# Kernel tuning notes

Hardware: AMD Instinct MI355X
Metric: run time of the kernel (lower is better)

The kernel has to match this reference:

```python
import jax, jax.numpy as jnp
import numpy as np

B, S, HIDDEN = 1, 2048, 3584
NH, NKV, HD = 16, 8, 256
N_REP = NH // NKV
EPS = 1e-6
SCALING = 256.0 ** -0.5  # query_pre_attn_scalar=256
SOFTCAP = 50.0
NEG = -1e9


def rmsnorm(x, w):
    # Gemma RMSNorm with unit offset, computed in fp32
    xf = x.astype(jnp.float32)
    n = xf * jax.lax.rsqrt(jnp.mean(xf * xf, axis=-1, keepdims=True) + EPS)
    return (n * (1.0 + w.astype(jnp.float32))).astype(x.dtype)


def rope(x, cos, sin):
    # x: [B,S,H,D]; gemma pairs (x[:D/2], x[D/2:]) as complex (rotate-half)
    x1, x2 = jnp.split(x, 2, axis=-1)
    c = cos[None, :, None, :]
    s = sin[None, :, None, :]
    return jnp.concatenate([x1 * c - x2 * s, x1 * s + x2 * c], axis=-1).astype(x.dtype)


def setup_inputs() -> dict:
    key = jax.random.key(0)
    ks = jax.random.split(key, 6)
    hidden_states = jax.random.normal(ks[0], (B, S, HIDDEN), jnp.float32)
    w_qkv = jax.random.normal(ks[1], ((NH + 2 * NKV) * HD, HIDDEN), jnp.float32) * 0.02
    w_o = jax.random.normal(ks[2], (HIDDEN, NH * HD), jnp.float32) * 0.02
    q_norm_w = jax.random.normal(ks[3], (HD,), jnp.float32) * 0.1
    k_norm_w = jax.random.normal(ks[4], (HD,), jnp.float32) * 0.1
    k_cache = jnp.zeros((B, S, NKV, HD), jnp.float32)
    v_cache = jnp.zeros((B, S, NKV, HD), jnp.float32)
    kv_write_indices = jnp.arange(S, dtype=jnp.int32)
    # rotary tables, theta=10000
    inv_freq = 1.0 / (10000.0 ** (np.arange(0, HD, 2, dtype=np.float32) / HD))
    t = np.arange(S, dtype=np.float32)
    freqs = np.outer(t, inv_freq)  # [S, HD/2]
    cos = jnp.asarray(np.cos(freqs), jnp.float32)
    sin = jnp.asarray(np.sin(freqs), jnp.float32)
    # causal additive mask [1,1,S,S]
    causal = np.tril(np.ones((S, S), dtype=bool))
    mask = jnp.asarray(np.where(causal, 0.0, NEG).astype(np.float32))[None, None]
    return {"hidden_states": hidden_states, "cos": cos, "sin": sin,
            "kv_write_indices": kv_write_indices, "k_cache": k_cache,
            "v_cache": v_cache, "mask": mask, "w_qkv": w_qkv, "w_o": w_o,
            "q_norm_w": q_norm_w, "k_norm_w": k_norm_w}


def reference(hidden_states, cos, sin, kv_write_indices, k_cache, v_cache,
              mask, w_qkv, w_o, q_norm_w, k_norm_w):
    qkv = jnp.einsum('bsh,oh->bso', hidden_states, w_qkv)
    q_size, kv_size = NH * HD, NKV * HD
    xq = qkv[..., :q_size].reshape(B, S, NH, HD)
    xk = qkv[..., q_size:q_size + kv_size].reshape(B, S, NKV, HD)
    xv = qkv[..., q_size + kv_size:].reshape(B, S, NKV, HD)
    xq = rmsnorm(xq, q_norm_w)
    xk = rmsnorm(xk, k_norm_w)
    xq = rope(xq, cos, sin)
    xk = rope(xk, cos, sin)
    # KV cache write (index_copy_ along dim 1)
    kc = k_cache.at[:, kv_write_indices].set(xk)
    vc = v_cache.at[:, kv_write_indices].set(xv)
    # GQA expand
    key = jnp.repeat(kc, N_REP, axis=2)   # [B,S,NH,HD]
    val = jnp.repeat(vc, N_REP, axis=2)
    q = xq.transpose(0, 2, 1, 3) * SCALING  # [B,NH,S,HD]
    k = key.transpose(0, 2, 1, 3)
    v = val.transpose(0, 2, 1, 3)
    scores = jnp.einsum('bhqd,bhkd->bhqk', q, k)
    scores = jnp.tanh(scores / SOFTCAP) * SOFTCAP  # logit softcapping
    scores = scores + mask
    p = jax.nn.softmax(scores, axis=-1)
    out = jnp.einsum('bhqk,bhkd->bhqd', p, v)
    out = out.transpose(0, 2, 1, 3).reshape(B, S, NH * HD)
    return jnp.einsum('bsd,hd->bsh', out, w_o)
```

## Files before the change

kernel.cpp:

```cpp
#include <hip/hip_runtime.h>

typedef __bf16 bf16;
typedef __bf16 bf16x4 __attribute__((ext_vector_type(4)));
typedef __bf16 bf16x8 __attribute__((ext_vector_type(8)));
typedef float f32x4 __attribute__((ext_vector_type(4)));

#define S_LEN 2048
#define HID   3584
#define NHEADS 16
#define NKVH   8
#define HDIM   256
#define QKV_O  8192
#define O_IN   4096

typedef const __attribute__((address_space(1))) void* gp_t;
typedef __attribute__((address_space(3))) void* sp_t;

__device__ __forceinline__ void async16(const void* g, void* s) {
  __builtin_amdgcn_global_load_lds((gp_t)g, (sp_t)s, 16, 0, 0);
}

__device__ __forceinline__ f32x4 mfma16(bf16x8 a, bf16x8 b, f32x4 c) {
  return __builtin_amdgcn_mfma_f32_16x16x32_bf16(a, b, c, 0, 0, 0);
}

__global__ __launch_bounds__(256) void cast_kernel(const float* __restrict__ in,
                                                   bf16* __restrict__ out, int n4) {
  int i = blockIdx.x * 256 + threadIdx.x;
  if (i >= n4) return;
  f32x4 v = ((const f32x4*)in)[i];
  bf16x4 o = { (bf16)v[0], (bf16)v[1], (bf16)v[2], (bf16)v[3] };
  ((bf16x4*)out)[i] = o;
}

__global__ __launch_bounds__(256) void add2_kernel(const float* __restrict__ a,
                                                   const float* __restrict__ b,
                                                   float* __restrict__ o, int n4) {
  int i = blockIdx.x * 256 + threadIdx.x;
  if (i >= n4) return;
  f32x4 x = ((const f32x4*)a)[i];
  f32x4 y = ((const f32x4*)b)[i];
  ((f32x4*)o)[i] = x + y;
}

#define GSTG(gb, lb, kk, half, LDAB) do {                              \
    const bf16* _g = (gb) + (size_t)((half) * 128) * (LDAB) + (kk);    \
    bf16* _l = (lb) + (half) * 128 * 64 + soff;                        \
    async16(_g, _l);                                                   \
    async16(_g + (size_t)64 * (LDAB), _l + 64 * 64);                   \
  } while (0)
#define LD12(ab, bb, cx, ar, br) do {                                  \
    const bf16* _pa = (ab) + arow;                                     \
    const bf16* _pb = (bb) + brow;                                     \
    _Pragma("unroll")                                                  \
    for (int _i = 0; _i < 8; _i++) ar[_i] = *(const bf16x8*)(_pa + _i * 16 * 64 + (cx)); \
    _Pragma("unroll")                                                  \
    for (int _j = 0; _j < 4; _j++) br[_j] = *(const bf16x8*)(_pb + _j * 16 * 64 + (cx)); \
  } while (0)
#define MM32(ar, br) do {                                              \
    __builtin_amdgcn_s_setprio(1);                                     \
    _Pragma("unroll")                                                  \
    for (int _i = 0; _i < 8; _i++)                                     \
      _Pragma("unroll")                                                \
      for (int _j = 0; _j < 4; _j++)                                   \
        acc[_i][_j] = mfma16(ar[_i], br[_j], acc[_i][_j]);             \
    __builtin_amdgcn_s_setprio(0);                                     \
  } while (0)
#define BARS() do { __builtin_amdgcn_s_barrier(); __builtin_amdgcn_sched_barrier(0); } while (0)
#define LGKM0() asm volatile("s_waitcnt lgkmcnt(0)" ::: "memory")
#define WAITV8() asm volatile("s_waitcnt vmcnt(8)" ::: "memory")

#define GEMM_PIPE_BODY(LDAB)                                           \
  f32x4 acc[8][4];                                                     \
  _Pragma("unroll")                                                    \
  for (int i = 0; i < 8; i++)                                          \
    _Pragma("unroll")                                                  \
    for (int j = 0; j < 4; j++) { f32x4 z = {0.f, 0.f, 0.f, 0.f}; acc[i][j] = z; } \
  bf16x8 a0[8], b0[4], a1[8], b1[4];                                   \
  const int nT = K >> 6;                                               \
  const int nIter = K >> 7;                                            \
  GSTG(Ag, As0, 0, 0, LDAB); GSTG(Ag, As0, 0, 1, LDAB);                \
  GSTG(Bg, Bs0, 0, 0, LDAB); GSTG(Bg, Bs0, 0, 1, LDAB);                \
  GSTG(Ag, As1, 64, 0, LDAB); GSTG(Ag, As1, 64, 1, LDAB);              \
  GSTG(Bg, Bs1, 64, 0, LDAB); GSTG(Bg, Bs1, 64, 1, LDAB);              \
  WAITV8();                                                            \
  BARS();                                                              \
  LD12(As0, Bs0, c0, a0, b0);                                          \
  for (int t = 0; t < nIter; t++) {                                    \
    int t2 = 2 * t + 2; if (t2 > nT - 1) t2 = nT - 1;                  \
    int t3 = 2 * t + 3; if (t3 > nT - 1) t3 = nT - 1;                  \
    int k2 = t2 * 64, k3 = t3 * 64;                                    \
              \
    LD12(As0, Bs0, c1, a1, b1);                                        \
    MM32(a0, b0);                                                      \
    LGKM0();                                                           \
    BARS();                                                            \
    \
    GSTG(Ag, As0, k2, 0, LDAB); GSTG(Ag, As0, k2, 1, LDAB);            \
    GSTG(Bg, Bs0, k2, 0, LDAB); GSTG(Bg, Bs0, k2, 1, LDAB);            \
    MM32(a1, b1);                                                      \
    WAITV8();                                                          \
    BARS();                                                            \
    LD12(As1, Bs1, c0, a0, b0);                                        \
                                             \
    LD12(As1, Bs1, c1, a1, b1);                                        \
    MM32(a0, b0);                                                      \
    LGKM0();                                                           \
    BARS();                                                            \
                                                              \
    GSTG(Ag, As1, k3, 0, LDAB); GSTG(Ag, As1, k3, 1, LDAB);            \
    GSTG(Bg, Bs1, k3, 0, LDAB); GSTG(Bg, Bs1, k3, 1, LDAB);            \
    MM32(a1, b1);                                                      \
    WAITV8();                                                          \
    BARS();                                                            \
    LD12(As0, Bs0, c0, a0, b0);                                        \
  }

__global__ __launch_bounds__(512, 2) void gemm_nt_8p(const bf16* __restrict__ A,
                                                     const bf16* __restrict__ B,
                                                     float* __restrict__ C,
                                                     int M, int N, int K) {
  __shared__ bf16 As0[256 * 64];
  __shared__ bf16 Bs0[256 * 64];
  __shared__ bf16 As1[256 * 64];
  __shared__ bf16 Bs1[256 * 64];
  int tid = threadIdx.x;
  int lane = tid & 63;
  int w = tid >> 6;
  int wm = w >> 2, wn = w & 3;
  int lid = blockIdx.x;
  int oid = (lid & 7) * 32 + (lid >> 3);
  int rect = oid >> 5, ri = oid & 31;
  int bm = (rect & 3) * 2 + (ri >> 4);
  int bn = (rect >> 2) * 16 + (ri & 15);
  int srow = tid >> 3, schunk = tid & 7;
  int gcol = (schunk ^ (srow & 7)) * 8;
  const bf16* Ag = A + (size_t)(bm * 256 + srow) * K + gcol;
  const bf16* Bg = B + (size_t)(bn * 256 + srow) * K + gcol;
  int soff = srow * 64 + schunk * 8;
  int fr = lane & 15, fq = lane >> 4;
  int c0 = ((fq) ^ (fr & 7)) * 8;
  int c1 = ((4 + fq) ^ (fr & 7)) * 8;
  const int arow = (wm * 128 + fr) * 64;
  const int brow = (wn * 64 + fr) * 64;

  GEMM_PIPE_BODY(K)

  int row0 = bm * 256 + wm * 128 + fq * 4;
  int col0 = bn * 256 + wn * 64 + fr;
#pragma unroll
  for (int i = 0; i < 8; i++)
#pragma unroll
    for (int j = 0; j < 4; j++)
#pragma unroll
      for (int r = 0; r < 4; r++)
        C[(size_t)(row0 + i * 16 + r) * N + col0 + j * 16] = acc[i][j][r];
}

__global__ __launch_bounds__(512, 2) void gemm_nt_8p_ks(const bf16* __restrict__ A,
                                                        const bf16* __restrict__ B,
                                                        float* __restrict__ C,
                                                        int M, int N, int K, int lda) {
  __shared__ bf16 As0[256 * 64];
  __shared__ bf16 Bs0[256 * 64];
  __shared__ bf16 As1[256 * 64];
  __shared__ bf16 Bs1[256 * 64];
  int tid = threadIdx.x;
  int lane = tid & 63;
  int w = tid >> 6;
  int wm = w >> 2, wn = w & 3;
  int lid = blockIdx.x;
  int ks = lid >= 112;
  int l2 = lid - ks * 112;
  int oid = (l2 & 7) * 14 + (l2 >> 3);
  int bm = oid / 14;
  int bn = oid - bm * 14;
  int kbase = ks * K;
  float* Cp = C + (size_t)ks * M * N;
  int srow = tid >> 3, schunk = tid & 7;
  int gcol = (schunk ^ (srow & 7)) * 8;
  const bf16* Ag = A + (size_t)(bm * 256 + srow) * lda + kbase + gcol;
  const bf16* Bg = B + (size_t)(bn * 256 + srow) * lda + kbase + gcol;
  int soff = srow * 64 + schunk * 8;
  int fr = lane & 15, fq = lane >> 4;
  int c0 = ((fq) ^ (fr & 7)) * 8;
  int c1 = ((4 + fq) ^ (fr & 7)) * 8;
  const int arow = (wm * 128 + fr) * 64;
  const int brow = (wn * 64 + fr) * 64;

  GEMM_PIPE_BODY(lda)

  int row0 = bm * 256 + wm * 128 + fq * 4;
  int col0 = bn * 256 + wn * 64 + fr;
#pragma unroll
  for (int i = 0; i < 8; i++)
#pragma unroll
    for (int j = 0; j < 4; j++)
#pragma unroll
      for (int r = 0; r < 4; r++)
        Cp[(size_t)(row0 + i * 16 + r) * N + col0 + j * 16] = acc[i][j][r];
}

__global__ __launch_bounds__(256) void qk_norm_rope(const float* __restrict__ qkv,
                                                    const float* __restrict__ cosb,
                                                    const float* __restrict__ sinb,
                                                    const float* __restrict__ qw,
                                                    const float* __restrict__ kw,
                                                    bf16* __restrict__ qout,
                                                    bf16* __restrict__ kout) {
  int s = blockIdx.x;
  int lane = threadIdx.x & 63;
  int w = threadIdx.x >> 6;
  int d0 = lane * 4;
  int dr = d0 & 127;
  f32x4 cv = *(const f32x4*)(cosb + s * 128 + dr);
  f32x4 sv = *(const f32x4*)(sinb + s * 128 + dr);
  bool hi = lane >= 32;
#pragma unroll
  for (int r = 0; r < 6; r++) {
    int head = r * 4 + w;
    const float* x = qkv + (size_t)s * QKV_O + head * HDIM + d0;
    f32x4 v = *(const f32x4*)x;
    float ss = v[0] * v[0] + v[1] * v[1] + v[2] * v[2] + v[3] * v[3];
#pragma unroll
    for (int off = 32; off > 0; off >>= 1) ss += __shfl_xor(ss, off);
    float scale = rsqrtf(ss * (1.0f / HDIM) + 1e-6f);
    bool isq = head < NHEADS;
    const float* wn = isq ? qw : kw;
    f32x4 wv = *(const f32x4*)(wn + d0);
    float y[4], o[4];
#pragma unroll
    for (int i = 0; i < 4; i++) y[i] = v[i] * scale * (1.0f + wv[i]);
#pragma unroll
    for (int i = 0; i < 4; i++) {
      float py = __shfl_xor(y[i], 32);
      o[i] = hi ? (py * sv[i] + y[i] * cv[i]) : (y[i] * cv[i] - py * sv[i]);
    }
    float mult = isq ? 0.0625f : 1.0f;
    bf16x4 ov = { (bf16)(o[0] * mult), (bf16)(o[1] * mult), (bf16)(o[2] * mult), (bf16)(o[3] * mult) };
    if (isq) *(bf16x4*)(qout + ((size_t)head * S_LEN + s) * HDIM + d0) = ov;
    else     *(bf16x4*)(kout + ((size_t)(head - NHEADS) * S_LEN + s) * HDIM + d0) = ov;
  }
}

__global__ __launch_bounds__(256) void v_transpose(const float* __restrict__ qkv, bf16* __restrict__ vt) {
  __shared__ float tile[64][65];
  int dt = blockIdx.x, st = blockIdx.y, h = blockIdx.z;
  int t = threadIdx.x;
  int d0 = dt * 64, s0 = st * 64;
#pragma unroll
  for (int i = 0; i < 16; i++) {
    int idx = i * 256 + t;
    int r = idx >> 6, c = idx & 63;
    tile[r][c] = qkv[(size_t)(s0 + r) * QKV_O + 6144 + h * HDIM + d0 + c];
  }
  __syncthreads();
#pragma unroll
  for (int i = 0; i < 16; i++) {
    int idx = i * 256 + t;
    int dr = idx >> 6, sc = idx & 63;
    vt[((size_t)h * HDIM + d0 + dr) * S_LEN + s0 + sc] = (bf16)tile[sc][dr];
  }
}

#define PSTRIDE 40
__global__ __launch_bounds__(256) void attn_kernel(const bf16* __restrict__ q,
                                                   const bf16* __restrict__ kx,
                                                   const bf16* __restrict__ vt,
                                                   bf16* __restrict__ aout) {
  __shared__ bf16 kt[32 * 256];
  __shared__ bf16 vtile[256 * 32];
  __shared__ bf16 pbuf[4][16 * PSTRIDE];
  int h = blockIdx.x;
  int y = blockIdx.y;
  int qt = (y < 16) ? y : 47 - y;
  int kvh = h >> 1;
  int tid = threadIdx.x;
  int lane = tid & 63, w = tid >> 6;
  int fr = lane & 15, fq = lane >> 4;
  int qs = qt * 64;
  bf16x8 qf[8];
  const bf16* qb = q + ((size_t)h * S_LEN + qs + w * 16 + fr) * HDIM + fq * 8;
#pragma unroll
  for (int i = 0; i < 8; i++) qf[i] = *(const bf16x8*)(qb + i * 32);
  f32x4 acc[16];
#pragma unroll
  for (int i = 0; i < 16; i++) { f32x4 z = {0.f, 0.f, 0.f, 0.f}; acc[i] = z; }
  float lsum[4] = {0.f, 0.f, 0.f, 0.f};
  int krow = w * 2 + (lane >> 5);
  int kcolr = (lane & 31) * 8;
  const bf16* kg = kx + (size_t)kvh * S_LEN * HDIM;
  int vd = w * 16 + (lane >> 2);
  int vsw = (vd >> 1) & 3;
  int vcl = (lane & 3) * 8;
  int vcg = (((lane & 3) ^ vsw) * 8);
  const bf16* vg = vt + (size_t)kvh * HDIM * S_LEN;
  int rot0 = (fq * 8 - fr * 8) & 255;
  int rot1 = (fq * 8 - fr * 8 - 128) & 255;
  const bf16* kt0 = &kt[fr * 256];
  const bf16* kt1 = &kt[(16 + fr) * 256];
  int fsw = (fr >> 1) & 3;
  int kmax = qs + 64;
  for (int k0 = 0; k0 < kmax; k0 += 32) {
    __syncthreads();
#pragma unroll
    for (int p = 0; p < 4; p++) {
      int r = p * 8 + krow;
      int gc = (kcolr + r * 8) & 255;
      async16(kg + (size_t)(k0 + r) * HDIM + gc, &kt[r * 256 + kcolr]);
      int d = p * 64 + vd;
      async16(vg + (size_t)d * S_LEN + k0 + vcg, &vtile[d * 32 + vcl]);
    }
    __syncthreads();
    f32x4 s0 = {0.f, 0.f, 0.f, 0.f}, s1 = {0.f, 0.f, 0.f, 0.f};
#pragma unroll
    for (int kk = 0; kk < 8; kk++) {
      bf16x8 b0 = *(const bf16x8*)(kt0 + ((kk * 32 + rot0) & 255));
      bf16x8 b1 = *(const bf16x8*)(kt1 + ((kk * 32 + rot1) & 255));
      s0 = mfma16(qf[kk], b0, s0);
      s1 = mfma16(qf[kk], b1, s1);
    }
#pragma unroll
    for (int reg = 0; reg < 4; reg++) {
      int rowg = qs + w * 16 + fq * 4 + reg;
      float u0 = __builtin_amdgcn_exp2f(0.057707802f * s0[reg]);
      float u1 = __builtin_amdgcn_exp2f(0.057707802f * s1[reg]);
      float p0 = __builtin_amdgcn_exp2f(28.853901f - 144.26950f * __builtin_amdgcn_rcpf(u0 + 1.0f));
      float p1 = __builtin_amdgcn_exp2f(28.853901f - 144.26950f * __builtin_amdgcn_rcpf(u1 + 1.0f));
      p0 = (k0 + fr <= rowg) ? p0 : 0.0f;
      p1 = (k0 + 16 + fr <= rowg) ? p1 : 0.0f;
      lsum[reg] += p0 + p1;
      pbuf[w][(fq * 4 + reg) * PSTRIDE + fr] = (bf16)p0;
      pbuf[w][(fq * 4 + reg) * PSTRIDE + 16 + fr] = (bf16)p1;
    }
    bf16x8 pf = *(const bf16x8*)&pbuf[w][fr * PSTRIDE + fq * 8];
#pragma unroll
    for (int ct = 0; ct < 16; ct++) {
      bf16x8 vf = *(const bf16x8*)&vtile[(ct * 16 + fr) * 32 + (fq ^ fsw) * 8];
      acc[ct] = mfma16(pf, vf, acc[ct]);
    }
  }
  float rl[4];
#pragma unroll
  for (int reg = 0; reg < 4; reg++) {
    float l = lsum[reg];
    l += __shfl_xor(l, 1);
    l += __shfl_xor(l, 2);
    l += __shfl_xor(l, 4);
    l += __shfl_xor(l, 8);
    rl[reg] = 1.0f / l;
  }
#pragma unroll
  for (int ct = 0; ct < 16; ct++)
#pragma unroll
    for (int reg = 0; reg < 4; reg++)
      aout[(size_t)(qs + w * 16 + fq * 4 + reg) * O_IN + h * HDIM + ct * 16 + fr] =
          (bf16)(acc[ct][reg] * rl[reg]);
}

extern "C" void kernel_launch(void* const* d_in, const int* in_sizes, int n_in,
                              void* d_out, int out_size, void* d_ws, size_t ws_size,
                              hipStream_t stream) {
  const float* hidden = (const float*)d_in[0];
  const float* cosb   = (const float*)d_in[1];
  const float* sinb   = (const float*)d_in[2];
  const float* wqkv   = (const float*)d_in[7];
  const float* wo     = (const float*)d_in[8];
  const float* qnw    = (const float*)d_in[9];
  const float* knw    = (const float*)d_in[10];
  float* out = (float*)d_out;
  char* ws = (char*)d_ws;
  bf16*  h_bf    = (bf16*)(ws + 0);
  bf16*  wqkv_bf = (bf16*)(ws + 14680064);
  bf16*  wo_bf   = (bf16*)(ws + 73400320);
  float* qkv     = (float*)(ws + 102760448);
  bf16*  qb      = (bf16*)(ws + 169869312);
  bf16*  kb      = (bf16*)(ws + 186646528);
  bf16*  vtb     = (bf16*)(ws + 195035136);
  bf16*  attnb   = (bf16*)(ws + 203423744);
  float* part0   = (float*)(ws + 102760448);
  float* part1   = part0 + (size_t)2048 * 3584;

  cast_kernel<<<7168, 256, 0, stream>>>(hidden, h_bf, 1835008);
  cast_kernel<<<28672, 256, 0, stream>>>(wqkv, wqkv_bf, 7340032);
  cast_kernel<<<14336, 256, 0, stream>>>(wo, wo_bf, 3670016);
  gemm_nt_8p<<<256, 512, 0, stream>>>(h_bf, wqkv_bf, qkv, 2048, 8192, 3584);
  qk_norm_rope<<<2048, 256, 0, stream>>>(qkv, cosb, sinb, qnw, knw, qb, kb);
  v_transpose<<<dim3(4, 32, 8), 256, 0, stream>>>(qkv, vtb);
  attn_kernel<<<dim3(16, 32), 256, 0, stream>>>(qb, kb, vtb, attnb);
  gemm_nt_8p_ks<<<224, 512, 0, stream>>>(attnb, wo_bf, part0, 2048, 3584, 2048, 4096);
  add2_kernel<<<7168, 256, 0, stream>>>(part0, part1, out, 1835008);
}
```

Measured before the change: 580.0 us.

## Double-buffer K/V tiles in attention kernel with async prefetch and MFMA priority

The attention kernel now keeps two LDS buffers for the K and V tiles. It issues the async global-to-LDS loads for the next 32-key block before computing on the current one, using a partial vmcnt wait to overlap memory with MFMA work. It also raises wave priority around the MFMA loops and requests two blocks per CU through launch_bounds. The cost is twice the LDS footprint per block, around 66KB, which may limit occupancy and conflicts with the two-blocks-per-CU target on a 160KB LDS CU. The hand-written waitcnt and barriers also risk ordering errors.

```diff
diff --git a/kernel.cpp b/kernel.cpp
--- a/kernel.cpp
+++ b/kernel.cpp
@@ -95,7 +95,7 @@
     MM32(a0, b0);                                                      \
     LGKM0();                                                           \
     BARS();                                                            \
-    \
+                                \
     GSTG(Ag, As0, k2, 0, LDAB); GSTG(Ag, As0, k2, 1, LDAB);            \
     GSTG(Bg, Bs0, k2, 0, LDAB); GSTG(Bg, Bs0, k2, 1, LDAB);            \
     MM32(a1, b1);                                                      \
@@ -264,12 +264,12 @@
 }
 
 #define PSTRIDE 40
-__global__ __launch_bounds__(256) void attn_kernel(const bf16* __restrict__ q,
-                                                   const bf16* __restrict__ kx,
-                                                   const bf16* __restrict__ vt,
-                                                   bf16* __restrict__ aout) {
-  __shared__ bf16 kt[32 * 256];
-  __shared__ bf16 vtile[256 * 32];
+__global__ __launch_bounds__(256, 2) void attn_kernel(const bf16* __restrict__ q,
+                                                      const bf16* __restrict__ kx,
+                                                      const bf16* __restrict__ vt,
+                                                      bf16* __restrict__ aout) {
+  __shared__ bf16 kt[2][32 * 256];
+  __shared__ bf16 vtile[2][256 * 32];
   __shared__ bf16 pbuf[4][16 * PSTRIDE];
   int h = blockIdx.x;
   int y = blockIdx.y;
@@ -297,22 +297,41 @@
   const bf16* vg = vt + (size_t)kvh * HDIM * S_LEN;
   int rot0 = (fq * 8 - fr * 8) & 255;
   int rot1 = (fq * 8 - fr * 8 - 128) & 255;
-  const bf16* kt0 = &kt[fr * 256];
-  const bf16* kt1 = &kt[(16 + fr) * 256];
   int fsw = (fr >> 1) & 3;
   int kmax = qs + 64;
-  for (int k0 = 0; k0 < kmax; k0 += 32) {
-    __syncthreads();
-#pragma unroll
-    for (int p = 0; p < 4; p++) {
-      int r = p * 8 + krow;
-      int gc = (kcolr + r * 8) & 255;
-      async16(kg + (size_t)(k0 + r) * HDIM + gc, &kt[r * 256 + kcolr]);
-      int d = p * 64 + vd;
-      async16(vg + (size_t)d * S_LEN + k0 + vcg, &vtile[d * 32 + vcl]);
+
+#define ASTG(KK, B) do {                                                   \
+    bf16* _kb = &kt[(B)][0]; bf16* _vb = &vtile[(B)][0];                   \
+    _Pragma("unroll")                                                      \
+    for (int p = 0; p < 4; p++) {                                          \
+      int r = p * 8 + krow;                                                \
+      int gc = (kcolr + r * 8) & 255;                                      \
+      async16(kg + (size_t)((KK) + r) * HDIM + gc, _kb + r * 256 + kcolr); \
+      int d = p * 64 + vd;                                                 \
+      async16(vg + (size_t)d * S_LEN + (KK) + vcg, _vb + d * 32 + vcl);    \
+    }                                                                      \
+  } while (0)
+
+  ASTG(0, 0);
+  int ib = 0;
+  for (int k0 = 0; k0 < kmax; k0 += 32, ib ^= 1) {
+    __builtin_amdgcn_s_barrier();
+    __builtin_amdgcn_sched_barrier(0);
+    if (k0 + 32 < kmax) {
+      ASTG(k0 + 32, ib ^ 1);
+      asm volatile("s_waitcnt vmcnt(8)" ::: "memory");
+    } else {
+      asm volatile("s_waitcnt vmcnt(0)" ::: "memory");
     }
-    __syncthreads();
+    __builtin_amdgcn_sched_barrier(0);
+    __builtin_amdgcn_s_barrier();
+    __builtin_amdgcn_sched_barrier(0);
+    const bf16* ktb = &kt[ib][0];
+    const bf16* vtb = &vtile[ib][0];
+    const bf16* kt0 = ktb + fr * 256;
+    const bf16* kt1 = ktb + (16 + fr) * 256;
     f32x4 s0 = {0.f, 0.f, 0.f, 0.f}, s1 = {0.f, 0.f, 0.f, 0.f};
+    __builtin_amdgcn_s_setprio(1);
 #pragma unroll
     for (int kk = 0; kk < 8; kk++) {
       bf16x8 b0 = *(const bf16x8*)(kt0 + ((kk * 32 + rot0) & 255));
@@ -320,6 +339,7 @@
       s0 = mfma16(qf[kk], b0, s0);
       s1 = mfma16(qf[kk], b1, s1);
     }
+    __builtin_amdgcn_s_setprio(0);
 #pragma unroll
     for (int reg = 0; reg < 4; reg++) {
       int rowg = qs + w * 16 + fq * 4 + reg;
@@ -334,12 +354,15 @@
       pbuf[w][(fq * 4 + reg) * PSTRIDE + 16 + fr] = (bf16)p1;
     }
     bf16x8 pf = *(const bf16x8*)&pbuf[w][fr * PSTRIDE + fq * 8];
+    __builtin_amdgcn_s_setprio(1);
 #pragma unroll
     for (int ct = 0; ct < 16; ct++) {
-      bf16x8 vf = *(const bf16x8*)&vtile[(ct * 16 + fr) * 32 + (fq ^ fsw) * 8];
+      bf16x8 vf = *(const bf16x8*)&vtb[(ct * 16 + fr) * 32 + (fq ^ fsw) * 8];
       acc[ct] = mfma16(pf, vf, acc[ct]);
     }
-  }
+    __builtin_amdgcn_s_setprio(0);
+  }
+#undef ASTG
   float rl[4];
 #pragma unroll
   for (int reg = 0; reg < 4; reg++) {
```

New measurement: 580.0 us. About the same (+0.0%).
